# Kernel tuning notes

Measured on AMD Instinct MI355X. Metric: run time of the kernel, lower is better.

The kernel has to match this reference:

```python
import jax, jax.numpy as jnp
import numpy as np

DIM = 1024
HEADS = 16
DIM_HEAD = 64
INNER = HEADS * DIM_HEAD  # 1024
SCALE = DIM_HEAD ** -0.5


def setup_inputs() -> dict:
    key = jax.random.key(0)
    k0, k1, k2 = jax.random.split(key, 3)
    x = jax.random.normal(k0, (4, 2048, DIM), dtype=jnp.float32)
    ln_gamma = jnp.ones((DIM,), dtype=jnp.float32)
    ln_beta = jnp.zeros((DIM,), dtype=jnp.float32)
    w_qkv = jax.random.normal(k1, (DIM, 3 * INNER), dtype=jnp.float32) * (DIM ** -0.5)
    w_out = jax.random.normal(k2, (INNER, DIM), dtype=jnp.float32) * (INNER ** -0.5)
    b_out = jnp.zeros((DIM,), dtype=jnp.float32)
    return {"x": x, "ln_gamma": ln_gamma, "ln_beta": ln_beta,
            "w_qkv": w_qkv, "w_out": w_out, "b_out": b_out}


def reference(x, ln_gamma, ln_beta, w_qkv, w_out, b_out):
    # LayerNorm over last dim (eps matches torch default 1e-5)
    mu = jnp.mean(x, axis=-1, keepdims=True)
    var = jnp.mean(jnp.square(x - mu), axis=-1, keepdims=True)
    xn = (x - mu) * jax.lax.rsqrt(var + 1e-5) * ln_gamma + ln_beta
    # QKV projection (no bias)
    qkv = xn @ w_qkv  # [b, t, 3*inner]
    q, k, v = jnp.split(qkv, 3, axis=-1)
    B, T, _ = x.shape
    def to_heads(t):
        return t.reshape(B, T, HEADS, DIM_HEAD).transpose(0, 2, 1, 3)  # b h t d
    q, k, v = to_heads(q), to_heads(k), to_heads(v)
    dots = jnp.einsum('bhid,bhjd->bhij', q, k) * SCALE
    attn = jax.nn.softmax(dots, axis=-1)
    out = jnp.einsum('bhij,bhjd->bhid', attn, v)
    out = out.transpose(0, 2, 1, 3).reshape(B, T, INNER)
    return out @ w_out + b_out
```

## Files before the change

### kernel.cpp

```cpp
#include <hip/hip_runtime.h>


#define DIMX 1024
#define TSEQ 2048
#define NB 4
#define NH 16
#define DH 64
#define NROWS (NB * TSEQ)
#define QSCALE 0.18033688011112042f

typedef __bf16 bf16_t;
typedef __bf16 bf16x8 __attribute__((ext_vector_type(8)));
typedef __bf16 bf16x4 __attribute__((ext_vector_type(4)));
typedef float f32x4 __attribute__((ext_vector_type(4)));

#if __has_builtin(__builtin_amdgcn_exp2f)
#define EXP2F __builtin_amdgcn_exp2f
#else
#define EXP2F exp2f
#endif

__device__ __forceinline__ bf16x4 cvt4(f32x4 v) {
    return __builtin_convertvector(v, bf16x4);
}
__device__ __forceinline__ void async16(const bf16_t* g, bf16_t* l) {
    __builtin_amdgcn_global_load_lds(
        (const __attribute__((address_space(1))) unsigned int*)g,
        (__attribute__((address_space(3))) unsigned int*)l, 16, 0, 0);
}

__global__ __launch_bounds__(256) void ln_kernel(
    const float* __restrict__ x, const float* __restrict__ g,
    const float* __restrict__ b, bf16_t* __restrict__ xn) {
    int row = blockIdx.x, tid = threadIdx.x;
    const float4 xv = *(const float4*)(x + (size_t)row * DIMX + tid * 4);
    float s = xv.x + xv.y + xv.z + xv.w;
    float q = xv.x * xv.x + xv.y * xv.y + xv.z * xv.z + xv.w * xv.w;
    for (int o = 32; o > 0; o >>= 1) {
        s += __shfl_xor(s, o);
        q += __shfl_xor(q, o);
    }
    __shared__ float2 red[4];
    int wave = tid >> 6, lane = tid & 63;
    if (lane == 0) red[wave] = make_float2(s, q);
    __syncthreads();
    float2 r0 = red[0], r1 = red[1], r2 = red[2], r3 = red[3];
    s = r0.x + r1.x + r2.x + r3.x;
    q = r0.y + r1.y + r2.y + r3.y;
    float mu = s * (1.0f / DIMX);
    float var = q * (1.0f / DIMX) - mu * mu;
    float rstd = rsqrtf(var + 1e-5f);
    float4 gv = *(const float4*)(g + tid * 4);
    float4 bv = *(const float4*)(b + tid * 4);
    f32x4 r;
    r[0] = (xv.x - mu) * rstd * gv.x + bv.x;
    r[1] = (xv.y - mu) * rstd * gv.y + bv.y;
    r[2] = (xv.z - mu) * rstd * gv.z + bv.z;
    r[3] = (xv.w - mu) * rstd * gv.w + bv.w;
    *(bf16x4*)(xn + (size_t)row * DIMX + tid * 4) = cvt4(r);
}

__global__ __launch_bounds__(256) void transpose_cast(
    const float* __restrict__ src, bf16_t* __restrict__ dst, int R, int C) {
    __shared__ float tile[32][33];
    int c0 = blockIdx.x * 32, r0 = blockIdx.y * 32;
    int tx = threadIdx.x, ty = threadIdx.y;
    for (int i = ty; i < 32; i += 8)
        tile[i][tx] = src[(size_t)(r0 + i) * C + c0 + tx];
    __syncthreads();
    for (int i = ty; i < 32; i += 8)
        dst[(size_t)(c0 + i) * R + r0 + tx] = (bf16_t)tile[tx][i];
}

#define MFMA16 __builtin_amdgcn_mfma_f32_16x16x32_bf16

template <int MODE>
__global__ __launch_bounds__(512, 2) void gemm256(
    const bf16_t* __restrict__ A, const bf16_t* __restrict__ BT,
    void* __restrict__ Cout, const float* __restrict__ bias, int M, int N, int K) {
    __shared__ __align__(16) bf16_t As[2][256 * 64];
    __shared__ __align__(16) bf16_t Bs[2][256 * 64];
    int tid = threadIdx.x, lane = tid & 63, wave = tid >> 6;
    int lm = lane & 15, quad = lane >> 4;
    int wr = wave >> 2, wc = wave & 3;

    int nbx = gridDim.x;
    int nwg = nbx * gridDim.y;
    int linear = blockIdx.y * nbx + blockIdx.x;
    int cpx = nwg >> 3;
    int swz = (linear & 7) * cpx + (linear >> 3);
    int bx = swz % nbx, by = swz / nbx;
    int m0 = by * 256, n0 = bx * 256;

    int srow = tid >> 3, sc8 = tid & 7;
    int scol = (sc8 ^ (srow & 7)) << 3;
    const bf16_t* ga = A + (size_t)(m0 + srow) * K + scol;
    const bf16_t* gb = BT + (size_t)(n0 + srow) * K + scol;
    int ldst = tid << 3;

    int sw0 = ((quad ^ (lm & 7)) << 3);
    int sw1 = (((4 + quad) ^ (lm & 7)) << 3);

    f32x4 zero = {0.f, 0.f, 0.f, 0.f};
    f32x4 acc[8][4];
#pragma unroll
    for (int i = 0; i < 8; ++i)
#pragma unroll
        for (int j = 0; j < 4; ++j) acc[i][j] = zero;

#pragma unroll
    for (int i = 0; i < 4; ++i) async16(ga + (size_t)i * 64 * K, &As[0][i * 4096 + ldst]);
#pragma unroll
    for (int i = 0; i < 4; ++i) async16(gb + (size_t)i * 64 * K, &Bs[0][i * 4096 + ldst]);
    asm volatile("s_waitcnt vmcnt(0)" ::: "memory");
    __builtin_amdgcn_s_barrier();

    int nkt = K >> 6;
    for (int kt = 0; kt < nkt; ++kt) {
        int c = kt & 1;
        int k1 = (kt + 1) << 6;
        bool pf = (kt + 1) < nkt;
        const bf16_t* pa = &As[c][0];
        const bf16_t* pb = &Bs[c][0];
        bf16_t* na = &As[c ^ 1][0];
        bf16_t* nb = &Bs[c ^ 1][0];
        bf16x8 af[4][2], bfr[2][2];

#pragma unroll
        for (int t = 0; t < 4; ++t) {
            int ro = (wr * 128 + t * 16 + lm) * 64;
            af[t][0] = *(const bf16x8*)&pa[ro + sw0];
            af[t][1] = *(const bf16x8*)&pa[ro + sw1];
        }
#pragma unroll
        for (int t = 0; t < 2; ++t) {
            int ro = (wc * 64 + t * 16 + lm) * 64;
            bfr[t][0] = *(const bf16x8*)&pb[ro + sw0];
            bfr[t][1] = *(const bf16x8*)&pb[ro + sw1];
        }
        if (pf) {
#pragma unroll
            for (int i = 0; i < 4; ++i)
                async16(ga + (size_t)i * 64 * K + k1, &na[i * 4096 + ldst]);
        }
        __builtin_amdgcn_s_barrier();
        asm volatile("s_waitcnt lgkmcnt(0)" ::: "memory");
        __builtin_amdgcn_s_setprio(1);
#pragma unroll
        for (int mt = 0; mt < 4; ++mt)
#pragma unroll
            for (int nt = 0; nt < 2; ++nt) {
                acc[mt][nt] = MFMA16(af[mt][0], bfr[nt][0], acc[mt][nt], 0, 0, 0);
                acc[mt][nt] = MFMA16(af[mt][1], bfr[nt][1], acc[mt][nt], 0, 0, 0);
            }
        __builtin_amdgcn_s_setprio(0);
        __builtin_amdgcn_s_barrier();

#pragma unroll
        for (int t = 0; t < 2; ++t) {
            int ro = (wc * 64 + (2 + t) * 16 + lm) * 64;
            bfr[t][0] = *(const bf16x8*)&pb[ro + sw0];
            bfr[t][1] = *(const bf16x8*)&pb[ro + sw1];
        }
        if (pf) {
#pragma unroll
            for (int i = 0; i < 4; ++i)
                async16(gb + (size_t)i * 64 * K + k1, &nb[i * 4096 + ldst]);
        }
        __builtin_amdgcn_s_barrier();
        asm volatile("s_waitcnt lgkmcnt(0)" ::: "memory");
        __builtin_amdgcn_s_setprio(1);
#pragma unroll
        for (int mt = 0; mt < 4; ++mt)
#pragma unroll
            for (int nt = 0; nt < 2; ++nt) {
                acc[mt][2 + nt] = MFMA16(af[mt][0], bfr[nt][0], acc[mt][2 + nt], 0, 0, 0);
                acc[mt][2 + nt] = MFMA16(af[mt][1], bfr[nt][1], acc[mt][2 + nt], 0, 0, 0);
            }
        __builtin_amdgcn_s_setprio(0);
        __builtin_amdgcn_s_barrier();

#pragma unroll
        for (int t = 0; t < 4; ++t) {
            int ro = (wr * 128 + (4 + t) * 16 + lm) * 64;
            af[t][0] = *(const bf16x8*)&pa[ro + sw0];
            af[t][1] = *(const bf16x8*)&pa[ro + sw1];
        }
        __builtin_amdgcn_s_barrier();
        asm volatile("s_waitcnt lgkmcnt(0)" ::: "memory");
        __builtin_amdgcn_s_setprio(1);
#pragma unroll
        for (int mt = 0; mt < 4; ++mt)
#pragma unroll
            for (int nt = 0; nt < 2; ++nt) {
                acc[4 + mt][2 + nt] = MFMA16(af[mt][0], bfr[nt][0], acc[4 + mt][2 + nt], 0, 0, 0);
                acc[4 + mt][2 + nt] = MFMA16(af[mt][1], bfr[nt][1], acc[4 + mt][2 + nt], 0, 0, 0);
            }
        __builtin_amdgcn_s_setprio(0);
        __builtin_amdgcn_s_barrier();

#pragma unroll
        for (int t = 0; t < 2; ++t) {
            int ro = (wc * 64 + t * 16 + lm) * 64;
            bfr[t][0] = *(const bf16x8*)&pb[ro + sw0];
            bfr[t][1] = *(const bf16x8*)&pb[ro + sw1];
        }
        __builtin_amdgcn_s_barrier();
        asm volatile("s_waitcnt lgkmcnt(0)" ::: "memory");
        __builtin_amdgcn_s_setprio(1);
#pragma unroll
        for (int mt = 0; mt < 4; ++mt)
#pragma unroll
            for (int nt = 0; nt < 2; ++nt) {
                acc[4 + mt][nt] = MFMA16(af[mt][0], bfr[nt][0], acc[4 + mt][nt], 0, 0, 0);
                acc[4 + mt][nt] = MFMA16(af[mt][1], bfr[nt][1], acc[4 + mt][nt], 0, 0, 0);
            }
        __builtin_amdgcn_s_setprio(0);
        asm volatile("s_waitcnt vmcnt(0)" ::: "memory");
        __builtin_amdgcn_s_barrier();
    }

#pragma unroll
    for (int mt = 0; mt < 8; ++mt) {
#pragma unroll
        for (int nt = 0; nt < 4; ++nt) {
            int m = m0 + wr * 128 + mt * 16 + quad * 4;
            int n = n0 + wc * 64 + nt * 16 + lm;
            if (MODE == 1) {
                int sel = n >> 10, nn = n & 1023, h = nn >> 6, d = nn & 63;
                int b = m >> 11, t = m & 2047;
                if (sel == 2) {
                    *(bf16x4*)((bf16_t*)Cout + (size_t)2 * 8388608 +
                               ((size_t)((b * NH + h) * DH + d)) * TSEQ + t) = cvt4(acc[mt][nt]);
                } else {
                    f32x4 sv = acc[mt][nt] * (sel == 0 ? QSCALE : 1.0f);
                    bf16x4 c4 = cvt4(sv);
#pragma unroll
                    for (int r = 0; r < 4; ++r)
                        ((bf16_t*)Cout)[(size_t)sel * 8388608 +
                                        ((size_t)((b * NH + h) * TSEQ + t + r)) * DH + d] = c4[r];
                }
            } else {
                float bn = bias[n];
#pragma unroll
                for (int r = 0; r < 4; ++r)
                    ((float*)Cout)[(size_t)(m + r) * N + n] = acc[mt][nt][r] + bn;
            }
        }
    }
}

__global__ __launch_bounds__(256, 2) void attn_mfma(
    const bf16_t* __restrict__ qkv, bf16_t* __restrict__ o) {
    int bh = blockIdx.y;
    int qt = blockIdx.x;
    const bf16_t* qb = qkv + (size_t)bh * TSEQ * DH;
    const bf16_t* kb = qkv + (size_t)8388608 + (size_t)bh * TSEQ * DH;
    const bf16_t* vb = qkv + (size_t)16777216 + (size_t)bh * DH * TSEQ;
    int tid = threadIdx.x, wave = tid >> 6, lane = tid & 63;
    int lm = lane & 15, quad = lane >> 4, lx = lm & 7;

    __shared__ __align__(16) bf16_t Ks[2][64 * 64];
    __shared__ __align__(16) bf16_t Vt[2][64 * 64];
    __shared__ __align__(16) bf16_t Ps[4 * 1024];

    int roff = tid >> 3;
    int cperm = ((tid & 7) ^ (roff & 7)) * 8;
    const bf16_t* kp0 = kb + (size_t)roff * DH + cperm;
    const bf16_t* kp1 = kb + (size_t)(32 + roff) * DH + cperm;
    const bf16_t* vp0 = vb + (size_t)roff * TSEQ + cperm;
    const bf16_t* vp1 = vb + (size_t)(32 + roff) * TSEQ + cperm;
    int l0 = tid * 8, l1 = (256 + tid) * 8;

    bf16x8 qf[4][2];
#pragma unroll
    for (int u = 0; u < 4; ++u)
#pragma unroll
        for (int ks = 0; ks < 2; ++ks)
            qf[u][ks] = *(const bf16x8*)(qb +
                (size_t)(qt * 256 + wave * 64 + u * 16 + lm) * DH + ks * 32 + quad * 8);

    f32x4 zero = {0.f, 0.f, 0.f, 0.f};
    f32x4 m16 = {-16.f, -16.f, -16.f, -16.f};
    f32x4 acc[4][4];
#pragma unroll
    for (int u = 0; u < 4; ++u)
#pragma unroll
        for (int dt = 0; dt < 4; ++dt) acc[u][dt] = zero;
    f32x4 l4[4] = {zero, zero, zero, zero};

    int fo0 = (quad ^ lx) * 8;
    int fo1 = ((4 + quad) ^ lx) * 8;
    int pb = wave * 1024 + lm * 64;

    async16(kp0, &Ks[0][l0]);
    async16(kp1, &Ks[0][l1]);
    async16(vp0, &Vt[0][l0]);
    async16(vp1, &Vt[0][l1]);
    kp0 += 64 * DH; kp1 += 64 * DH; vp0 += 64; vp1 += 64;
    asm volatile("s_waitcnt vmcnt(0)" ::: "memory");
    __builtin_amdgcn_s_barrier();

    for (int jt = 0; jt < TSEQ / 64; ++jt) {
        int c = jt & 1;
        if (jt + 1 < TSEQ / 64) {
            async16(kp0, &Ks[c ^ 1][l0]);
            async16(kp1, &Ks[c ^ 1][l1]);
            async16(vp0, &Vt[c ^ 1][l0]);
            async16(vp1, &Vt[c ^ 1][l1]);
            kp0 += 64 * DH; kp1 += 64 * DH; vp0 += 64; vp1 += 64;
        }

        bf16x8 kf[4][2];
#pragma unroll
        for (int nt = 0; nt < 4; ++nt) {
            kf[nt][0] = *(const bf16x8*)&Ks[c][(nt * 16 + lm) * 64 + fo0];
            kf[nt][1] = *(const bf16x8*)&Ks[c][(nt * 16 + lm) * 64 + fo1];
        }

        bf16x8 pf[4][2];
#pragma unroll
        for (int u = 0; u < 4; ++u) {
            f32x4 s[4];
#pragma unroll
            for (int nt = 0; nt < 4; ++nt) {
                s[nt] = __builtin_amdgcn_mfma_f32_16x16x32_bf16(kf[nt][0], qf[u][0], m16, 0, 0, 0);
                s[nt] = __builtin_amdgcn_mfma_f32_16x16x32_bf16(kf[nt][1], qf[u][1], s[nt], 0, 0, 0);
            }
#pragma unroll
            for (int nt = 0; nt < 4; ++nt) {
                f32x4 p;
#pragma unroll
                for (int e = 0; e < 4; ++e) p[e] = EXP2F(s[nt][e]);
                l4[u] += p;
                *(bf16x4*)&Ps[pb + ((nt * 2 + (quad >> 1)) ^ lx) * 8 + (quad & 1) * 4] = cvt4(p);
            }
            pf[u][0] = *(const bf16x8*)&Ps[pb + fo0];
            pf[u][1] = *(const bf16x8*)&Ps[pb + fo1];
        }

#pragma unroll
        for (int dt = 0; dt < 4; ++dt) {
            bf16x8 vf0 = *(const bf16x8*)&Vt[c][(dt * 16 + lm) * 64 + fo0];
            bf16x8 vf1 = *(const bf16x8*)&Vt[c][(dt * 16 + lm) * 64 + fo1];
#pragma unroll
            for (int u = 0; u < 4; ++u) {
                acc[u][dt] = __builtin_amdgcn_mfma_f32_16x16x32_bf16(vf0, pf[u][0], acc[u][dt], 0, 0, 0);
                acc[u][dt] = __builtin_amdgcn_mfma_f32_16x16x32_bf16(vf1, pf[u][1], acc[u][dt], 0, 0, 0);
            }
        }

        asm volatile("s_waitcnt vmcnt(0)" ::: "memory");
        __builtin_amdgcn_s_barrier();
    }

    int b = bh >> 4, h = bh & 15;
#pragma unroll
    for (int u = 0; u < 4; ++u) {
        float l = (l4[u][0] + l4[u][1]) + (l4[u][2] + l4[u][3]);
        l += __shfl_xor(l, 16);
        l += __shfl_xor(l, 32);
        float rl = 1.0f / l;
        int t = qt * 256 + wave * 64 + u * 16 + lm;
#pragma unroll
        for (int dt = 0; dt < 4; ++dt) {
            f32x4 ov = acc[u][dt] * rl;
            *(bf16x4*)(o + ((size_t)(b * TSEQ + t)) * DIMX + h * DH + dt * 16 + quad * 4) = cvt4(ov);
        }
    }
}

extern "C" void kernel_launch(void* const* d_in, const int* in_sizes, int n_in,
                              void* d_out, int out_size, void* d_ws, size_t ws_size,
                              hipStream_t stream) {
    const float* x = (const float*)d_in[0];
    const float* g = (const float*)d_in[1];
    const float* be = (const float*)d_in[2];
    const float* w_qkv = (const float*)d_in[3];
    const float* w_out = (const float*)d_in[4];
    const float* b_out = (const float*)d_in[5];
    float* out = (float*)d_out;
    char* ws = (char*)d_ws;

    bf16_t* xn = (bf16_t*)(ws);
    bf16_t* wqkvT = (bf16_t*)(ws + 16777216);
    bf16_t* woutT = (bf16_t*)(ws + 23068672);
    bf16_t* qkv = (bf16_t*)(ws + 25165824);
    bf16_t* attno = (bf16_t*)(ws + 75497472);

    ln_kernel<<<NROWS, 256, 0, stream>>>(x, g, be, xn);
    transpose_cast<<<dim3(96, 32), dim3(32, 8), 0, stream>>>(w_qkv, wqkvT, 1024, 3072);
    transpose_cast<<<dim3(32, 32), dim3(32, 8), 0, stream>>>(w_out, woutT, 1024, 1024);
    gemm256<1><<<dim3(12, 32), 512, 0, stream>>>(xn, wqkvT, (void*)qkv, nullptr, NROWS, 3072, 1024);
    attn_mfma<<<dim3(8, 64), 256, 0, stream>>>(qkv, attno);
    gemm256<2><<<dim3(4, 32), 512, 0, stream>>>(attno, woutT, (void*)out, b_out, NROWS, 1024, 1024);
}
```

Measured before the change: 286.0 us.

## Split attention block across 8 waves and add MFMA priority hints

The attention kernel now launches 512 threads per block. Each of 8 waves handles 32 query rows instead of 64, and each thread issues one async K/V load per tile instead of two. The goal is more waves to hide latency and fewer registers per wave, giving higher occupancy (launch bounds 512,4). s_setprio is raised around the MFMA sections so matrix work is favoured over the exp/LDS phases. The cost is that each wave re-reads the K/V fragments from LDS for fewer query rows, and the per-wave P buffer in LDS doubles.

```diff
diff --git a/kernel.cpp b/kernel.cpp
--- a/kernel.cpp
+++ b/kernel.cpp
@@ -250,7 +250,7 @@
     }
 }
 
-__global__ __launch_bounds__(256, 2) void attn_mfma(
+__global__ __launch_bounds__(512, 4) void attn_mfma(
     const bf16_t* __restrict__ qkv, bf16_t* __restrict__ o) {
     int bh = blockIdx.y;
     int qt = blockIdx.x;
@@ -262,53 +262,47 @@
 
     __shared__ __align__(16) bf16_t Ks[2][64 * 64];
     __shared__ __align__(16) bf16_t Vt[2][64 * 64];
-    __shared__ __align__(16) bf16_t Ps[4 * 1024];
+    __shared__ __align__(16) bf16_t Ps[8 * 1024];
 
     int roff = tid >> 3;
     int cperm = ((tid & 7) ^ (roff & 7)) * 8;
-    const bf16_t* kp0 = kb + (size_t)roff * DH + cperm;
-    const bf16_t* kp1 = kb + (size_t)(32 + roff) * DH + cperm;
-    const bf16_t* vp0 = vb + (size_t)roff * TSEQ + cperm;
-    const bf16_t* vp1 = vb + (size_t)(32 + roff) * TSEQ + cperm;
-    int l0 = tid * 8, l1 = (256 + tid) * 8;
-
-    bf16x8 qf[4][2];
-#pragma unroll
-    for (int u = 0; u < 4; ++u)
+    const bf16_t* kp = kb + (size_t)roff * DH + cperm;
+    const bf16_t* vp = vb + (size_t)roff * TSEQ + cperm;
+    int l0 = tid * 8;
+
+    bf16x8 qf[2][2];
+#pragma unroll
+    for (int u = 0; u < 2; ++u)
 #pragma unroll
         for (int ks = 0; ks < 2; ++ks)
             qf[u][ks] = *(const bf16x8*)(qb +
-                (size_t)(qt * 256 + wave * 64 + u * 16 + lm) * DH + ks * 32 + quad * 8);
+                (size_t)(qt * 256 + wave * 32 + u * 16 + lm) * DH + ks * 32 + quad * 8);
 
     f32x4 zero = {0.f, 0.f, 0.f, 0.f};
     f32x4 m16 = {-16.f, -16.f, -16.f, -16.f};
-    f32x4 acc[4][4];
-#pragma unroll
-    for (int u = 0; u < 4; ++u)
+    f32x4 acc[2][4];
+#pragma unroll
+    for (int u = 0; u < 2; ++u)
 #pragma unroll
         for (int dt = 0; dt < 4; ++dt) acc[u][dt] = zero;
-    f32x4 l4[4] = {zero, zero, zero, zero};
+    f32x4 l4[2] = {zero, zero};
 
     int fo0 = (quad ^ lx) * 8;
     int fo1 = ((4 + quad) ^ lx) * 8;
     int pb = wave * 1024 + lm * 64;
 
-    async16(kp0, &Ks[0][l0]);
-    async16(kp1, &Ks[0][l1]);
-    async16(vp0, &Vt[0][l0]);
-    async16(vp1, &Vt[0][l1]);
-    kp0 += 64 * DH; kp1 += 64 * DH; vp0 += 64; vp1 += 64;
+    async16(kp, &Ks[0][l0]);
+    async16(vp, &Vt[0][l0]);
+    kp += 64 * DH; vp += 64;
     asm volatile("s_waitcnt vmcnt(0)" ::: "memory");
     __builtin_amdgcn_s_barrier();
 
     for (int jt = 0; jt < TSEQ / 64; ++jt) {
         int c = jt & 1;
         if (jt + 1 < TSEQ / 64) {
-            async16(kp0, &Ks[c ^ 1][l0]);
-            async16(kp1, &Ks[c ^ 1][l1]);
-            async16(vp0, &Vt[c ^ 1][l0]);
-            async16(vp1, &Vt[c ^ 1][l1]);
-            kp0 += 64 * DH; kp1 += 64 * DH; vp0 += 64; vp1 += 64;
+            async16(kp, &Ks[c ^ 1][l0]);
+            async16(vp, &Vt[c ^ 1][l0]);
+            kp += 64 * DH; vp += 64;
         }
 
         bf16x8 kf[4][2];
@@ -318,15 +312,17 @@
             kf[nt][1] = *(const bf16x8*)&Ks[c][(nt * 16 + lm) * 64 + fo1];
         }
 
-        bf16x8 pf[4][2];
-#pragma unroll
-        for (int u = 0; u < 4; ++u) {
+        bf16x8 pf[2][2];
+#pragma unroll
+        for (int u = 0; u < 2; ++u) {
             f32x4 s[4];
+            __builtin_amdgcn_s_setprio(1);
 #pragma unroll
             for (int nt = 0; nt < 4; ++nt) {
                 s[nt] = __builtin_amdgcn_mfma_f32_16x16x32_bf16(kf[nt][0], qf[u][0], m16, 0, 0, 0);
                 s[nt] = __builtin_amdgcn_mfma_f32_16x16x32_bf16(kf[nt][1], qf[u][1], s[nt], 0, 0, 0);
             }
+            __builtin_amdgcn_s_setprio(0);
 #pragma unroll
             for (int nt = 0; nt < 4; ++nt) {
                 f32x4 p;
@@ -339,16 +335,18 @@
             pf[u][1] = *(const bf16x8*)&Ps[pb + fo1];
         }
 
+        __builtin_amdgcn_s_setprio(1);
 #pragma unroll
         for (int dt = 0; dt < 4; ++dt) {
             bf16x8 vf0 = *(const bf16x8*)&Vt[c][(dt * 16 + lm) * 64 + fo0];
             bf16x8 vf1 = *(const bf16x8*)&Vt[c][(dt * 16 + lm) * 64 + fo1];
 #pragma unroll
-            for (int u = 0; u < 4; ++u) {
+            for (int u = 0; u < 2; ++u) {
                 acc[u][dt] = __builtin_amdgcn_mfma_f32_16x16x32_bf16(vf0, pf[u][0], acc[u][dt], 0, 0, 0);
                 acc[u][dt] = __builtin_amdgcn_mfma_f32_16x16x32_bf16(vf1, pf[u][1], acc[u][dt], 0, 0, 0);
             }
         }
+        __builtin_amdgcn_s_setprio(0);
 
         asm volatile("s_waitcnt vmcnt(0)" ::: "memory");
         __builtin_amdgcn_s_barrier();
@@ -356,12 +354,12 @@
 
     int b = bh >> 4, h = bh & 15;
 #pragma unroll
-    for (int u = 0; u < 4; ++u) {
+    for (int u = 0; u < 2; ++u) {
         float l = (l4[u][0] + l4[u][1]) + (l4[u][2] + l4[u][3]);
         l += __shfl_xor(l, 16);
         l += __shfl_xor(l, 32);
         float rl = 1.0f / l;
-        int t = qt * 256 + wave * 64 + u * 16 + lm;
+        int t = qt * 256 + wave * 32 + u * 16 + lm;
 #pragma unroll
         for (int dt = 0; dt < 4; ++dt) {
             f32x4 ov = acc[u][dt] * rl;
@@ -392,6 +390,6 @@
     transpose_cast<<<dim3(96, 32), dim3(32, 8), 0, stream>>>(w_qkv, wqkvT, 1024, 3072);
     transpose_cast<<<dim3(32, 32), dim3(32, 8), 0, stream>>>(w_out, woutT, 1024, 1024);
     gemm256<1><<<dim3(12, 32), 512, 0, stream>>>(xn, wqkvT, (void*)qkv, nullptr, NROWS, 3072, 1024);
-    attn_mfma<<<dim3(8, 64), 256, 0, stream>>>(qkv, attno);
+    attn_mfma<<<dim3(8, 64), 512, 0, stream>>>(qkv, attno);
     gemm256<2><<<dim3(4, 32), 512, 0, stream>>>(attno, woutT, (void*)out, b_out, NROWS, 1024, 1024);
 }
```

New measurement: 290.0 us. No clear change (+1.4%).
